# Kernel optimization log

Measured on AMD Instinct MI355X. Metric: run time of the kernel, lower is better.

The kernel has to match this reference:

```python
import jax, jax.numpy as jnp
import numpy as np

N, E, D, L = 50000, 600000, 128, 3  # nodes, edges, feature dim, GIN layers
BN_EPS = 1e-5


def setup_inputs() -> dict:
    key = jax.random.key(0)
    ks = jax.random.split(key, 10)
    x = jax.random.normal(ks[0], (N, D), jnp.float32)
    edge_index = jax.random.randint(ks[1], (2, E), 0, N, jnp.int32)
    s = 1.0 / np.sqrt(D).astype(np.float32)
    W1 = jax.random.uniform(ks[2], (L, D, D), jnp.float32, -s, s)
    b1 = jax.random.uniform(ks[3], (L, D), jnp.float32, -s, s)
    W2 = jax.random.uniform(ks[4], (L, D, D), jnp.float32, -s, s)
    b2 = jax.random.uniform(ks[5], (L, D), jnp.float32, -s, s)
    gamma = jnp.ones((L, D), jnp.float32)
    beta = jnp.zeros((L, D), jnp.float32)
    fc_w = jax.random.uniform(ks[6], (D, 1), jnp.float32, -s, s)
    fc_b = jax.random.uniform(ks[7], (1,), jnp.float32, -s, s)
    return dict(x=x, edge_index=edge_index, W1=W1, b1=b1, W2=W2, b2=b2,
                gamma=gamma, beta=beta, fc_w=fc_w, fc_b=fc_b)


def reference(x, edge_index, W1, b1, W2, b2, gamma, beta, fc_w, fc_b):
    src, dst = edge_index[0], edge_index[1]
    h = x
    for l in range(L):
        # GINConv (eps=0): MLP(x_i + sum_{j->i} x_j)  -- gather then scatter-add
        agg = jax.ops.segment_sum(h[src], dst, num_segments=N)  # [N, D]
        z = h + agg
        z = jax.nn.relu(z @ W1[l] + b1[l]) @ W2[l] + b2[l]  # 2-layer MLP
        # BatchNorm1d (training mode: batch stats, biased variance)
        mu = z.mean(axis=0)
        var = z.var(axis=0)
        z = (z - mu) * jax.lax.rsqrt(var + BN_EPS) * gamma[l] + beta[l]
        h = jax.nn.relu(z)
    return h @ fc_w + fc_b  # [N, 1] per-node q-values
```

## Files before the change

kernel.cpp:

```cpp
#include <hip/hip_runtime.h>
#include <math.h>

#define NN 50000
#define NE 600000
#define DIM 128
#define LAYERS 3
#define BN_EPS 1e-5f

#define SC_ELE 2048
#define NSCAN ((NN + SC_ELE - 1) / SC_ELE)
#define TM 32

__global__ void k_init(int* __restrict__ deg, float* __restrict__ bnstats) {
    int i = blockIdx.x * 256 + threadIdx.x;
    if (i < NN) deg[i] = 0;
    if (i < LAYERS * 2 * DIM) bnstats[i] = 0.0f;
}

__global__ void k_hist(const int* __restrict__ dst, int* __restrict__ deg) {
    int e = blockIdx.x * 256 + threadIdx.x;
    if (e < NE) atomicAdd(&deg[dst[e]], 1);
}

__global__ __launch_bounds__(1024) void k_scan1(const int* __restrict__ deg,
                                                int* __restrict__ part,
                                                int* __restrict__ bsum) {
    __shared__ int ws[16];
    const int t = threadIdx.x, lane = t & 63, wv = t >> 6;
    const int base = blockIdx.x * SC_ELE;
    const int e0 = base + 2 * t, e1 = e0 + 1;
    const int v0 = (e0 < NN) ? deg[e0] : 0;
    const int v1 = (e1 < NN) ? deg[e1] : 0;
    const int s = v0 + v1;
    int incl = s;
    #pragma unroll
    for (int o = 1; o < 64; o <<= 1) {
        int u = __shfl_up(incl, o);
        if (lane >= o) incl += u;
    }
    if (lane == 63) ws[wv] = incl;
    __syncthreads();
    if (wv == 0) {
        int x = (lane < 16) ? ws[lane] : 0;
        int ix = x;
        #pragma unroll
        for (int o = 1; o < 16; o <<= 1) {
            int u = __shfl_up(ix, o);
            if (lane >= o) ix += u;
        }
        if (lane < 16) ws[lane] = ix - x;
        if (lane == 15) bsum[blockIdx.x] = ix;
    }
    __syncthreads();
    const int excl = incl - s + ws[wv];
    if (e0 < NN) part[e0] = excl;
    if (e1 < NN) part[e1] = excl + v0;
}

__global__ void k_scan2(const int* __restrict__ bsum, int* __restrict__ boff) {
    const int lane = threadIdx.x;
    const int v = (lane < NSCAN) ? bsum[lane] : 0;
    int ix = v;
    #pragma unroll
    for (int o = 1; o < 64; o <<= 1) {
        int u = __shfl_up(ix, o);
        if (lane >= o) ix += u;
    }
    if (lane < NSCAN) boff[lane] = ix - v;
}

__global__ void k_scan3(const int* __restrict__ part, const int* __restrict__ boff,
                        int* __restrict__ off, int* __restrict__ cur) {
    int i = blockIdx.x * 256 + threadIdx.x;
    if (i < NN) {
        int o = part[i] + boff[i >> 11];
        off[i] = o;
        cur[i] = o;
        if (i == 0) off[NN] = NE;
    }
}

__global__ void k_fill(const int* __restrict__ src, const int* __restrict__ dst,
                       int* __restrict__ cur, int* __restrict__ csr) {
    int e = blockIdx.x * 256 + threadIdx.x;
    if (e < NE) {
        int p = atomicAdd(&cur[dst[e]], 1);
        csr[p] = src[e];
    }
}

__global__ void k_fin(const float* __restrict__ bnsum, const float* __restrict__ bnsq,
                      const float* __restrict__ gamma, const float* __restrict__ beta,
                      float* __restrict__ scsh) {
    int j = threadIdx.x;
    const float invN = 1.0f / (float)NN;
    float mu  = bnsum[j] * invN;
    float var = bnsq[j] * invN - mu * mu;
    float k   = rsqrtf(var + BN_EPS) * gamma[j];
    scsh[j]       = k;
    scsh[DIM + j] = beta[j] - mu * k;
}

template <int NORM>
__global__ __launch_bounds__(256, 4) void k_layer(
        const float* __restrict__ hprev, const float* __restrict__ scsh,
        const int* __restrict__ off, const int* __restrict__ csr,
        const float* __restrict__ W1, const float* __restrict__ b1,
        const float* __restrict__ W2, const float* __restrict__ b2,
        float* __restrict__ zout,
        float* __restrict__ bnsum, float* __restrict__ bnsq) {
    __shared__ float zt[TM][DIM];
    const int t = threadIdx.x;
    const int lane = t & 63, wv = t >> 6;
    const int c = t & 31;
    const int r = t >> 5;
    const int row0 = blockIdx.x * TM;

    {
        float2 scv, shv;
        if (NORM) {
            scv = *(const float2*)&scsh[lane * 2];
            shv = *(const float2*)&scsh[DIM + lane * 2];
        }
        #pragma unroll
        for (int nb = 0; nb < 8; ++nb) {
            const int row = wv * 8 + nb;
            const int n = row0 + row;
            float2 acc = make_float2(0.f, 0.f);
            if (n < NN) {
                float2 v = *(const float2*)&hprev[(size_t)n * DIM + lane * 2];
                if (NORM) {
                    v.x = fmaxf(fmaf(v.x, scv.x, shv.x), 0.f);
                    v.y = fmaxf(fmaf(v.y, scv.y, shv.y), 0.f);
                }
                acc = v;
                const int end = off[n + 1];
                int i = off[n];
                for (; i + 1 < end; i += 2) {
                    int s0 = csr[i], s1 = csr[i + 1];
                    float2 v0 = *(const float2*)&hprev[(size_t)s0 * DIM + lane * 2];
                    float2 v1 = *(const float2*)&hprev[(size_t)s1 * DIM + lane * 2];
                    if (NORM) {
                        v0.x = fmaxf(fmaf(v0.x, scv.x, shv.x), 0.f);
                        v0.y = fmaxf(fmaf(v0.y, scv.y, shv.y), 0.f);
                        v1.x = fmaxf(fmaf(v1.x, scv.x, shv.x), 0.f);
                        v1.y = fmaxf(fmaf(v1.y, scv.y, shv.y), 0.f);
                    }
                    acc.x += v0.x + v1.x;
                    acc.y += v0.y + v1.y;
                }
                if (i < end) {
                    int s0 = csr[i];
                    float2 v0 = *(const float2*)&hprev[(size_t)s0 * DIM + lane * 2];
                    if (NORM) {
                        v0.x = fmaxf(fmaf(v0.x, scv.x, shv.x), 0.f);
                        v0.y = fmaxf(fmaf(v0.y, scv.y, shv.y), 0.f);
                    }
                    acc.x += v0.x;
                    acc.y += v0.y;
                }
            }
            *(float2*)&zt[row][lane * 2] = acc;
        }
    }
    __syncthreads();

    float acc[4][4];
    #pragma unroll
    for (int i = 0; i < 4; ++i)
        #pragma unroll
        for (int j = 0; j < 4; ++j) acc[i][j] = 0.0f;

    for (int k = 0; k < DIM; k += 4) {
        float4 a4[4];
        #pragma unroll
        for (int i = 0; i < 4; ++i) a4[i] = *(const float4*)&zt[r * 4 + i][k];
        #pragma unroll
        for (int kk = 0; kk < 4; ++kk) {
            const float4 b = *(const float4*)&W1[(k + kk) * DIM + c * 4];
            #pragma unroll
            for (int i = 0; i < 4; ++i) {
                const float a = (&a4[i].x)[kk];
                acc[i][0] = fmaf(a, b.x, acc[i][0]);
                acc[i][1] = fmaf(a, b.y, acc[i][1]);
                acc[i][2] = fmaf(a, b.z, acc[i][2]);
                acc[i][3] = fmaf(a, b.w, acc[i][3]);
            }
        }
    }
    __syncthreads();

    const float4 bias1 = *(const float4*)&b1[c * 4];
    #pragma unroll
    for (int i = 0; i < 4; ++i) {
        float4 y;
        y.x = fmaxf(acc[i][0] + bias1.x, 0.f);
        y.y = fmaxf(acc[i][1] + bias1.y, 0.f);
        y.z = fmaxf(acc[i][2] + bias1.z, 0.f);
        y.w = fmaxf(acc[i][3] + bias1.w, 0.f);
        *(float4*)&zt[r * 4 + i][c * 4] = y;
    }
    __syncthreads();

    #pragma unroll
    for (int i = 0; i < 4; ++i)
        #pragma unroll
        for (int j = 0; j < 4; ++j) acc[i][j] = 0.0f;

    for (int k = 0; k < DIM; k += 4) {
        float4 a4[4];
        #pragma unroll
        for (int i = 0; i < 4; ++i) a4[i] = *(const float4*)&zt[r * 4 + i][k];
        #pragma unroll
        for (int kk = 0; kk < 4; ++kk) {
            const float4 b = *(const float4*)&W2[(k + kk) * DIM + c * 4];
            #pragma unroll
            for (int i = 0; i < 4; ++i) {
                const float a = (&a4[i].x)[kk];
                acc[i][0] = fmaf(a, b.x, acc[i][0]);
                acc[i][1] = fmaf(a, b.y, acc[i][1]);
                acc[i][2] = fmaf(a, b.z, acc[i][2]);
                acc[i][3] = fmaf(a, b.w, acc[i][3]);
            }
        }
    }
    __syncthreads();

    const float4 bias2 = *(const float4*)&b2[c * 4];
    float s[4] = {0.f, 0.f, 0.f, 0.f};
    float q[4] = {0.f, 0.f, 0.f, 0.f};
    #pragma unroll
    for (int i = 0; i < 4; ++i) {
        int g = row0 + r * 4 + i;
        float4 zv;
        zv.x = acc[i][0] + bias2.x;
        zv.y = acc[i][1] + bias2.y;
        zv.z = acc[i][2] + bias2.z;
        zv.w = acc[i][3] + bias2.w;
        if (g < NN) {
            *(float4*)&zout[(size_t)g * DIM + c * 4] = zv;
            s[0] += zv.x; s[1] += zv.y; s[2] += zv.z; s[3] += zv.w;
            q[0] += zv.x * zv.x; q[1] += zv.y * zv.y;
            q[2] += zv.z * zv.z; q[3] += zv.w * zv.w;
        }
    }
    float* scratch = &zt[0][0];
    #pragma unroll
    for (int j = 0; j < 4; ++j) {
        scratch[r * DIM + c * 4 + j]        = s[j];
        scratch[1024 + r * DIM + c * 4 + j] = q[j];
    }
    __syncthreads();
    if (t < DIM) {
        float ss = 0.f, qq = 0.f;
        #pragma unroll
        for (int rr = 0; rr < 8; ++rr) {
            ss += scratch[rr * DIM + t];
            qq += scratch[1024 + rr * DIM + t];
        }
        atomicAdd(&bnsum[t], ss);
        atomicAdd(&bnsq[t], qq);
    }
}

__global__ __launch_bounds__(256) void k_fc(const float* __restrict__ z,
                                            const float* __restrict__ scsh,
                                            const float* __restrict__ fc_w,
                                            const float* __restrict__ fc_b,
                                            float* __restrict__ out) {
    int wid  = (blockIdx.x * 256 + threadIdx.x) >> 6;
    int lane = threadIdx.x & 63;
    if (wid >= NN) return;
    float2 v = *(const float2*)&z[(size_t)wid * DIM + lane * 2];
    float2 scv = *(const float2*)&scsh[lane * 2];
    float2 shv = *(const float2*)&scsh[DIM + lane * 2];
    v.x = fmaxf(fmaf(v.x, scv.x, shv.x), 0.f);
    v.y = fmaxf(fmaf(v.y, scv.y, shv.y), 0.f);
    float2 wv = *(const float2*)&fc_w[lane * 2];
    float s = v.x * wv.x + v.y * wv.y;
    #pragma unroll
    for (int o = 32; o >= 1; o >>= 1) s += __shfl_down(s, o);
    if (lane == 0) out[wid] = s + fc_b[0];
}

extern "C" void kernel_launch(void* const* d_in, const int* in_sizes, int n_in,
                              void* d_out, int out_size, void* d_ws, size_t ws_size,
                              hipStream_t stream) {
    const float* x     = (const float*)d_in[0];
    const int*   src   = (const int*)d_in[1];
    const int*   dst   = ((const int*)d_in[1]) + NE;
    const float* W1    = (const float*)d_in[2];
    const float* b1    = (const float*)d_in[3];
    const float* W2    = (const float*)d_in[4];
    const float* b2    = (const float*)d_in[5];
    const float* gamma = (const float*)d_in[6];
    const float* beta  = (const float*)d_in[7];
    const float* fc_w  = (const float*)d_in[8];
    const float* fc_b  = (const float*)d_in[9];
    float* out = (float*)d_out;

    char* ws = (char*)d_ws;
    size_t o = 0;
    auto carve = [&](size_t bytes) {
        char* p = ws + o;
        o += (bytes + 15) & ~(size_t)15;
        return p;
    };
    int*   deg     = (int*)carve(NN * 4);
    int*   off     = (int*)carve((NN + 1) * 4);
    int*   cur     = (int*)carve(NN * 4);
    int*   csr     = (int*)carve(NE * 4);
    int*   part    = (int*)carve(NN * 4);
    int*   bsum    = (int*)carve(NSCAN * 4);
    int*   boff    = (int*)carve(NSCAN * 4);
    float* bnstats = (float*)carve(LAYERS * 2 * DIM * 4);
    float* scsh    = (float*)carve(LAYERS * 2 * DIM * 4);
    float* zA      = (float*)carve((size_t)NN * DIM * 4);
    float* zB      = (float*)carve((size_t)NN * DIM * 4);

    k_init<<<(NN + 255) / 256, 256, 0, stream>>>(deg, bnstats);
    k_hist<<<(NE + 255) / 256, 256, 0, stream>>>(dst, deg);
    k_scan1<<<NSCAN, 1024, 0, stream>>>(deg, part, bsum);
    k_scan2<<<1, 64, 0, stream>>>(bsum, boff);
    k_scan3<<<(NN + 255) / 256, 256, 0, stream>>>(part, boff, off, cur);
    k_fill<<<(NE + 255) / 256, 256, 0, stream>>>(src, dst, cur, csr);

    const int nblk = (NN + TM - 1) / TM;
    float* zbuf[2] = {zA, zB};
    for (int l = 0; l < LAYERS; ++l) {
        const float* hin = (l == 0) ? x : zbuf[(l + 1) & 1];
        float* zo = zbuf[l & 1];
        float* sum_l = bnstats + l * DIM;
        float* sq_l  = bnstats + LAYERS * DIM + l * DIM;
        float* scsh_prev = scsh + (l - 1) * 2 * DIM;
        if (l == 0)
            k_layer<0><<<nblk, 256, 0, stream>>>(hin, nullptr, off, csr,
                                                 W1, b1, W2, b2, zo, sum_l, sq_l);
        else
            k_layer<1><<<nblk, 256, 0, stream>>>(hin, scsh_prev, off, csr,
                                                 W1 + (size_t)l * DIM * DIM, b1 + l * DIM,
                                                 W2 + (size_t)l * DIM * DIM, b2 + l * DIM,
                                                 zo, sum_l, sq_l);
        k_fin<<<1, 128, 0, stream>>>(sum_l, sq_l, gamma + l * DIM, beta + l * DIM,
                                     scsh + l * 2 * DIM);
    }

    k_fc<<<(NN * 64 + 255) / 256, 256, 0, stream>>>(zbuf[(LAYERS + 1) & 1],
                                                    scsh + (LAYERS - 1) * 2 * DIM,
                                                    fc_w, fc_b, out);
}
```

Baseline: 642.5 us.

## Split fused gather+MLP layer kernel into separate aggregation and MLP kernels

Each layer's fused kernel, which gathered neighbours into shared memory and then ran the MLP, becomes two kernels. One wave-per-node kernel does the aggregation and writes to global memory, then an in-place MLP kernel reads it back. The BN finalize kernel is removed and its scale/shift is computed inline in the aggregation and FC kernels. This aims to get more parallelism and latency hiding for the irregular gather, which had been limited by the MLP kernel's occupancy. The cost is an extra full write and read of the N×D activations per layer.

```diff
diff --git a/kernel.cpp b/kernel.cpp
--- a/kernel.cpp
+++ b/kernel.cpp
@@ -89,79 +89,88 @@
     }
 }
 
-__global__ void k_fin(const float* __restrict__ bnsum, const float* __restrict__ bnsq,
-                      const float* __restrict__ gamma, const float* __restrict__ beta,
-                      float* __restrict__ scsh) {
-    int j = threadIdx.x;
-    const float invN = 1.0f / (float)NN;
-    float mu  = bnsum[j] * invN;
-    float var = bnsq[j] * invN - mu * mu;
-    float k   = rsqrtf(var + BN_EPS) * gamma[j];
-    scsh[j]       = k;
-    scsh[DIM + j] = beta[j] - mu * k;
-}
-
 template <int NORM>
-__global__ __launch_bounds__(256, 4) void k_layer(
-        const float* __restrict__ hprev, const float* __restrict__ scsh,
-        const int* __restrict__ off, const int* __restrict__ csr,
-        const float* __restrict__ W1, const float* __restrict__ b1,
-        const float* __restrict__ W2, const float* __restrict__ b2,
-        float* __restrict__ zout,
-        float* __restrict__ bnsum, float* __restrict__ bnsq) {
+__global__ __launch_bounds__(256) void k_agg(const float* __restrict__ h,
+                                             const float* __restrict__ bnsum,
+                                             const float* __restrict__ bnsq,
+                                             const float* __restrict__ gamma,
+                                             const float* __restrict__ beta,
+                                             const int* __restrict__ off,
+                                             const int* __restrict__ csr,
+                                             float* __restrict__ a) {
+    int wid  = (blockIdx.x * 256 + threadIdx.x) >> 6;
+    int lane = threadIdx.x & 63;
+    if (wid >= NN) return;
+
+    float2 scv = make_float2(1.f, 0.f), shv = make_float2(0.f, 0.f);
+    if (NORM) {
+        const int j0 = lane * 2;
+        const float invN = 1.0f / (float)NN;
+        float mu0 = bnsum[j0] * invN;
+        float mu1 = bnsum[j0 + 1] * invN;
+        float k0 = rsqrtf(bnsq[j0] * invN - mu0 * mu0 + BN_EPS) * gamma[j0];
+        float k1 = rsqrtf(bnsq[j0 + 1] * invN - mu1 * mu1 + BN_EPS) * gamma[j0 + 1];
+        scv = make_float2(k0, k1);
+        shv = make_float2(beta[j0] - mu0 * k0, beta[j0 + 1] - mu1 * k1);
+    }
+
+    const int start = off[wid], end = off[wid + 1];
+    float2 v = *(const float2*)&h[(size_t)wid * DIM + lane * 2];
+    float2 acc;
+    if (NORM) {
+        acc.x = fmaxf(fmaf(v.x, scv.x, shv.x), 0.f);
+        acc.y = fmaxf(fmaf(v.y, scv.y, shv.y), 0.f);
+    } else {
+        acc = v;
+    }
+    int i = start;
+    for (; i + 1 < end; i += 2) {
+        int s0 = csr[i], s1 = csr[i + 1];
+        float2 v0 = *(const float2*)&h[(size_t)s0 * DIM + lane * 2];
+        float2 v1 = *(const float2*)&h[(size_t)s1 * DIM + lane * 2];
+        if (NORM) {
+            v0.x = fmaxf(fmaf(v0.x, scv.x, shv.x), 0.f);
+            v0.y = fmaxf(fmaf(v0.y, scv.y, shv.y), 0.f);
+            v1.x = fmaxf(fmaf(v1.x, scv.x, shv.x), 0.f);
+            v1.y = fmaxf(fmaf(v1.y, scv.y, shv.y), 0.f);
+        }
+        acc.x += v0.x + v1.x;
+        acc.y += v0.y + v1.y;
+    }
+    if (i < end) {
+        int s0 = csr[i];
+        float2 v0 = *(const float2*)&h[(size_t)s0 * DIM + lane * 2];
+        if (NORM) {
+            v0.x = fmaxf(fmaf(v0.x, scv.x, shv.x), 0.f);
+            v0.y = fmaxf(fmaf(v0.y, scv.y, shv.y), 0.f);
+        }
+        acc.x += v0.x;
+        acc.y += v0.y;
+    }
+    *(float2*)&a[(size_t)wid * DIM + lane * 2] = acc;
+}
+
+__global__ __launch_bounds__(256, 4) void k_mlp(float* __restrict__ z,
+                                                const float* __restrict__ W1,
+                                                const float* __restrict__ b1,
+                                                const float* __restrict__ W2,
+                                                const float* __restrict__ b2,
+                                                float* __restrict__ bnsum,
+                                                float* __restrict__ bnsq) {
     __shared__ float zt[TM][DIM];
     const int t = threadIdx.x;
-    const int lane = t & 63, wv = t >> 6;
     const int c = t & 31;
     const int r = t >> 5;
     const int row0 = blockIdx.x * TM;
 
-    {
-        float2 scv, shv;
-        if (NORM) {
-            scv = *(const float2*)&scsh[lane * 2];
-            shv = *(const float2*)&scsh[DIM + lane * 2];
-        }
-        #pragma unroll
-        for (int nb = 0; nb < 8; ++nb) {
-            const int row = wv * 8 + nb;
-            const int n = row0 + row;
-            float2 acc = make_float2(0.f, 0.f);
-            if (n < NN) {
-                float2 v = *(const float2*)&hprev[(size_t)n * DIM + lane * 2];
-                if (NORM) {
-                    v.x = fmaxf(fmaf(v.x, scv.x, shv.x), 0.f);
-                    v.y = fmaxf(fmaf(v.y, scv.y, shv.y), 0.f);
-                }
-                acc = v;
-                const int end = off[n + 1];
-                int i = off[n];
-                for (; i + 1 < end; i += 2) {
-                    int s0 = csr[i], s1 = csr[i + 1];
-                    float2 v0 = *(const float2*)&hprev[(size_t)s0 * DIM + lane * 2];
-                    float2 v1 = *(const float2*)&hprev[(size_t)s1 * DIM + lane * 2];
-                    if (NORM) {
-                        v0.x = fmaxf(fmaf(v0.x, scv.x, shv.x), 0.f);
-                        v0.y = fmaxf(fmaf(v0.y, scv.y, shv.y), 0.f);
-                        v1.x = fmaxf(fmaf(v1.x, scv.x, shv.x), 0.f);
-                        v1.y = fmaxf(fmaf(v1.y, scv.y, shv.y), 0.f);
-                    }
-                    acc.x += v0.x + v1.x;
-                    acc.y += v0.y + v1.y;
-                }
-                if (i < end) {
-                    int s0 = csr[i];
-                    float2 v0 = *(const float2*)&hprev[(size_t)s0 * DIM + lane * 2];
-                    if (NORM) {
-                        v0.x = fmaxf(fmaf(v0.x, scv.x, shv.x), 0.f);
-                        v0.y = fmaxf(fmaf(v0.y, scv.y, shv.y), 0.f);
-                    }
-                    acc.x += v0.x;
-                    acc.y += v0.y;
-                }
-            }
-            *(float2*)&zt[row][lane * 2] = acc;
-        }
+    #pragma unroll
+    for (int i = 0; i < 4; ++i) {
+        int f4 = t + i * 256;
+        int rr = f4 >> 5, c4 = f4 & 31;
+        int g  = row0 + rr;
+        float4 v = make_float4(0.f, 0.f, 0.f, 0.f);
+        if (g < NN) v = *(const float4*)&z[(size_t)g * DIM + c4 * 4];
+        *(float4*)&zt[rr][c4 * 4] = v;
     }
     __syncthreads();
 
@@ -238,7 +247,7 @@
         zv.z = acc[i][2] + bias2.z;
         zv.w = acc[i][3] + bias2.w;
         if (g < NN) {
-            *(float4*)&zout[(size_t)g * DIM + c * 4] = zv;
+            *(float4*)&z[(size_t)g * DIM + c * 4] = zv;
             s[0] += zv.x; s[1] += zv.y; s[2] += zv.z; s[3] += zv.w;
             q[0] += zv.x * zv.x; q[1] += zv.y * zv.y;
             q[2] += zv.z * zv.z; q[3] += zv.w * zv.w;
@@ -264,18 +273,28 @@
 }
 
 __global__ __launch_bounds__(256) void k_fc(const float* __restrict__ z,
-                                            const float* __restrict__ scsh,
+                                            const float* __restrict__ bnsum,
+                                            const float* __restrict__ bnsq,
+                                            const float* __restrict__ gamma,
+                                            const float* __restrict__ beta,
                                             const float* __restrict__ fc_w,
                                             const float* __restrict__ fc_b,
                                             float* __restrict__ out) {
     int wid  = (blockIdx.x * 256 + threadIdx.x) >> 6;
     int lane = threadIdx.x & 63;
     if (wid >= NN) return;
+    const int j0 = lane * 2;
+    const float invN = 1.0f / (float)NN;
+    float mu0 = bnsum[j0] * invN;
+    float mu1 = bnsum[j0 + 1] * invN;
+    float k0 = rsqrtf(bnsq[j0] * invN - mu0 * mu0 + BN_EPS) * gamma[j0];
+    float k1 = rsqrtf(bnsq[j0 + 1] * invN - mu1 * mu1 + BN_EPS) * gamma[j0 + 1];
+    float sh0 = beta[j0] - mu0 * k0;
+    float sh1 = beta[j0 + 1] - mu1 * k1;
+
     float2 v = *(const float2*)&z[(size_t)wid * DIM + lane * 2];
-    float2 scv = *(const float2*)&scsh[lane * 2];
-    float2 shv = *(const float2*)&scsh[DIM + lane * 2];
-    v.x = fmaxf(fmaf(v.x, scv.x, shv.x), 0.f);
-    v.y = fmaxf(fmaf(v.y, scv.y, shv.y), 0.f);
+    v.x = fmaxf(fmaf(v.x, k0, sh0), 0.f);
+    v.y = fmaxf(fmaf(v.y, k1, sh1), 0.f);
     float2 wv = *(const float2*)&fc_w[lane * 2];
     float s = v.x * wv.x + v.y * wv.y;
     #pragma unroll
@@ -314,7 +333,6 @@
     int*   bsum    = (int*)carve(NSCAN * 4);
     int*   boff    = (int*)carve(NSCAN * 4);
     float* bnstats = (float*)carve(LAYERS * 2 * DIM * 4);
-    float* scsh    = (float*)carve(LAYERS * 2 * DIM * 4);
     float* zA      = (float*)carve((size_t)NN * DIM * 4);
     float* zB      = (float*)carve((size_t)NN * DIM * 4);
 
@@ -325,27 +343,34 @@
     k_scan3<<<(NN + 255) / 256, 256, 0, stream>>>(part, boff, off, cur);
     k_fill<<<(NE + 255) / 256, 256, 0, stream>>>(src, dst, cur, csr);
 
-    const int nblk = (NN + TM - 1) / TM;
+    const int nblk_mlp = (NN + TM - 1) / TM;
+    const int nblk_agg = (NN * 64 + 255) / 256;
     float* zbuf[2] = {zA, zB};
     for (int l = 0; l < LAYERS; ++l) {
         const float* hin = (l == 0) ? x : zbuf[(l + 1) & 1];
         float* zo = zbuf[l & 1];
         float* sum_l = bnstats + l * DIM;
         float* sq_l  = bnstats + LAYERS * DIM + l * DIM;
-        float* scsh_prev = scsh + (l - 1) * 2 * DIM;
+        const float* sum_p = bnstats + (l - 1) * DIM;
+        const float* sq_p  = bnstats + LAYERS * DIM + (l - 1) * DIM;
         if (l == 0)
-            k_layer<0><<<nblk, 256, 0, stream>>>(hin, nullptr, off, csr,
-                                                 W1, b1, W2, b2, zo, sum_l, sq_l);
+            k_agg<0><<<nblk_agg, 256, 0, stream>>>(hin, nullptr, nullptr, nullptr,
+                                                   nullptr, off, csr, zo);
         else
-            k_layer<1><<<nblk, 256, 0, stream>>>(hin, scsh_prev, off, csr,
-                                                 W1 + (size_t)l * DIM * DIM, b1 + l * DIM,
-                                                 W2 + (size_t)l * DIM * DIM, b2 + l * DIM,
-                                                 zo, sum_l, sq_l);
-        k_fin<<<1, 128, 0, stream>>>(sum_l, sq_l, gamma + l * DIM, beta + l * DIM,
-                                     scsh + l * 2 * DIM);
+            k_agg<1><<<nblk_agg, 256, 0, stream>>>(hin, sum_p, sq_p,
+                                                   gamma + (l - 1) * DIM,
+                                                   beta + (l - 1) * DIM,
+                                                   off, csr, zo);
+        k_mlp<<<nblk_mlp, 256, 0, stream>>>(zo,
+                                            W1 + (size_t)l * DIM * DIM, b1 + l * DIM,
+                                            W2 + (size_t)l * DIM * DIM, b2 + l * DIM,
+                                            sum_l, sq_l);
     }
 
     k_fc<<<(NN * 64 + 255) / 256, 256, 0, stream>>>(zbuf[(LAYERS + 1) & 1],
-                                                    scsh + (LAYERS - 1) * 2 * DIM,
+                                                    bnstats + (LAYERS - 1) * DIM,
+                                                    bnstats + (2 * LAYERS - 1) * DIM,
+                                                    gamma + (LAYERS - 1) * DIM,
+                                                    beta + (LAYERS - 1) * DIM,
                                                     fc_w, fc_b, out);
 }
```

Result: faster. 608.2 us (-5.3%).
